# Optimization experiments

Hardware: AMD Instinct MI355X
Metric: run time of the kernel (lower is better)

Reference implementation:

```python
import jax, jax.numpy as jnp
import numpy as np

B, W, H = 16384, 16, 16
NUM_CLASSES = 1024
EMBED = 4
OUT = 1024

def setup_inputs() -> dict:
    key = jax.random.key(0)
    k0, k1, k2 = jax.random.split(key, 3)
    x = jax.random.randint(k0, (B, W, H), 0, NUM_CLASSES, dtype=jnp.int32)
    W_embed = jax.random.normal(k1, (NUM_CLASSES, EMBED), dtype=jnp.float32) * 0.02
    b_embed = jnp.zeros((EMBED,), dtype=jnp.float32)
    W_dense = jax.random.normal(k2, (EMBED * W * H, OUT), dtype=jnp.float32) * 0.02
    b_dense = jnp.zeros((OUT,), dtype=jnp.float32)
    return {"x": x, "W_embed": W_embed, "b_embed": b_embed, "W_dense": W_dense, "b_dense": b_dense}

def reference(x, W_embed, b_embed, W_dense, b_dense):
    # one_hot(x, C) @ W_embed + b_embed is mathematically a row-gather of W_embed
    emb = W_embed[x] + b_embed                 # (B, W, H, EMBED)
    flat = emb.reshape(emb.shape[0], -1)        # (B, W*H*EMBED)  == rearrange '... w h c -> ... (w h c)'
    return flat @ W_dense + b_dense             # (B, OUT)
```

## Files before the change

### kernel.cpp

```cpp
#include <hip/hip_runtime.h>
#include <stdint.h>
#include <stddef.h>

typedef __attribute__((ext_vector_type(8))) short bf16x8;
typedef __attribute__((ext_vector_type(4))) float f32x4;

typedef const __attribute__((address_space(1))) void* gptr1_t;
typedef __attribute__((address_space(3))) void* lptr3_t;

#define GLOAD_LDS16(gp, lp) \
  __builtin_amdgcn_global_load_lds((gptr1_t)(gp), (lptr3_t)(lp), 16, 0, 0)

__device__ __forceinline__ uint16_t f2bf(float f) {
  uint32_t u = __builtin_bit_cast(uint32_t, f);
  u += 0x7fffu + ((u >> 16) & 1u);
  return (uint16_t)(u >> 16);
}

#define MB   16384
#define NP   256
#define EMB  4
#define KDIM 1024
#define NDIM 1024

__global__ void build_a_kernel(const int* __restrict__ x,
                               const float* __restrict__ We,
                               const float* __restrict__ be,
                               uint16_t* __restrict__ A) {
  const int t = blockIdx.x * 256 + threadIdx.x;
  const int cls = x[t];
  const float4 e  = *(const float4*)(We + (size_t)cls * 4);
  const float4 bb = *(const float4*)be;
  ushort4 o;
  o.x = f2bf(e.x + bb.x);
  o.y = f2bf(e.y + bb.y);
  o.z = f2bf(e.z + bb.z);
  o.w = f2bf(e.w + bb.w);
  *(ushort4*)(A + (size_t)t * 4) = o;
}

__global__ void build_bt_kernel(const float* __restrict__ Wd,
                                uint16_t* __restrict__ Bt) {
  __shared__ uint16_t tile[32][33];
  const int k0 = blockIdx.y * 32;
  const int n0 = blockIdx.x * 32;
  const int tx = threadIdx.x;
  const int ty = threadIdx.y;
  #pragma unroll
  for (int r = 0; r < 32; r += 8)
    tile[ty + r][tx] = f2bf(Wd[(size_t)(k0 + ty + r) * NDIM + n0 + tx]);
  __syncthreads();
  #pragma unroll
  for (int r = 0; r < 32; r += 8)
    Bt[(size_t)(n0 + ty + r) * KDIM + k0 + tx] = tile[tx][ty + r];
}

#define BM 128
#define BN 128
#define BK 32

__global__ __launch_bounds__(256) void gemm_bt_kernel(
    const uint16_t* __restrict__ A,
    const uint16_t* __restrict__ Bt,
    const float* __restrict__ bias,
    float* __restrict__ C) {
  __shared__ uint16_t As[BM * BK];
  __shared__ uint16_t Bs[BN * BK];

  const int tid  = threadIdx.x;
  const int bm   = blockIdx.x;
  const int bn   = blockIdx.y;
  const int wave = tid >> 6;
  const int lane = tid & 63;
  const int wr   = wave >> 1;
  const int wc   = wave & 1;
  const int lm   = lane & 15;
  const int q    = lane >> 4;

  const int row0 = bm * BM;
  const int col0 = bn * BN;

  const int srow = tid >> 2;
  const int scol = (tid & 3) * 8;

  f32x4 acc[4][4];
  #pragma unroll
  for (int i = 0; i < 4; i++)
    #pragma unroll
    for (int j = 0; j < 4; j++)
      acc[i][j] = (f32x4){0.f, 0.f, 0.f, 0.f};

  for (int kt = 0; kt < KDIM / BK; ++kt) {
    const int k0 = kt * BK;
    GLOAD_LDS16(A  + (size_t)(row0      + srow) * KDIM + k0 + scol, As + tid * 8);
    GLOAD_LDS16(A  + (size_t)(row0 + 64 + srow) * KDIM + k0 + scol, As + 2048 + tid * 8);
    GLOAD_LDS16(Bt + (size_t)(col0      + srow) * KDIM + k0 + scol, Bs + tid * 8);
    GLOAD_LDS16(Bt + (size_t)(col0 + 64 + srow) * KDIM + k0 + scol, Bs + 2048 + tid * 8);
    __syncthreads();

    bf16x8 af[4], bfr[4];
    #pragma unroll
    for (int i = 0; i < 4; i++)
      af[i] = *(const bf16x8*)(As + (wr * 64 + i * 16 + lm) * BK + q * 8);
    #pragma unroll
    for (int j = 0; j < 4; j++)
      bfr[j] = *(const bf16x8*)(Bs + (wc * 64 + j * 16 + lm) * BK + q * 8);

    #pragma unroll
    for (int i = 0; i < 4; i++)
      #pragma unroll
      for (int j = 0; j < 4; j++)
        acc[i][j] = __builtin_amdgcn_mfma_f32_16x16x32_bf16(af[i], bfr[j], acc[i][j], 0, 0, 0);

    __syncthreads();
  }

  float bvals[4];
  #pragma unroll
  for (int j = 0; j < 4; j++)
    bvals[j] = bias[col0 + wc * 64 + j * 16 + lm];

  #pragma unroll
  for (int i = 0; i < 4; i++) {
    const int rbase = row0 + wr * 64 + i * 16 + q * 4;
    #pragma unroll
    for (int j = 0; j < 4; j++) {
      const int col = col0 + wc * 64 + j * 16 + lm;
      #pragma unroll
      for (int r = 0; r < 4; r++)
        C[(size_t)(rbase + r) * NDIM + col] = acc[i][j][r] + bvals[j];
    }
  }
}

__global__ void naive_kernel(const int* __restrict__ x,
                             const float* __restrict__ We,
                             const float* __restrict__ be,
                             const float* __restrict__ Wd,
                             const float* __restrict__ bd,
                             float* __restrict__ out) {
  __shared__ float emb[KDIM];
  const int b = blockIdx.x;
  const int tid = threadIdx.x;
  {
    const int cls = x[(size_t)b * NP + tid];
    const float4 e  = *(const float4*)(We + (size_t)cls * 4);
    const float4 bb = *(const float4*)be;
    emb[tid * 4 + 0] = e.x + bb.x;
    emb[tid * 4 + 1] = e.y + bb.y;
    emb[tid * 4 + 2] = e.z + bb.z;
    emb[tid * 4 + 3] = e.w + bb.w;
  }
  __syncthreads();
  float acc0 = bd[tid], acc1 = bd[tid + 256], acc2 = bd[tid + 512], acc3 = bd[tid + 768];
  for (int k = 0; k < KDIM; ++k) {
    const float a = emb[k];
    const float* w = Wd + (size_t)k * NDIM + tid;
    acc0 += a * w[0];
    acc1 += a * w[256];
    acc2 += a * w[512];
    acc3 += a * w[768];
  }
  float* o = out + (size_t)b * NDIM + tid;
  o[0] = acc0; o[256] = acc1; o[512] = acc2; o[768] = acc3;
}

extern "C" void kernel_launch(void* const* d_in, const int* in_sizes, int n_in,
                              void* d_out, int out_size, void* d_ws, size_t ws_size,
                              hipStream_t stream) {
  const int*   x  = (const int*)d_in[0];
  const float* We = (const float*)d_in[1];
  const float* be = (const float*)d_in[2];
  const float* Wd = (const float*)d_in[3];
  const float* bd = (const float*)d_in[4];
  float* out = (float*)d_out;

  const size_t needA = (size_t)MB * KDIM * sizeof(uint16_t);
  const size_t needB = (size_t)NDIM * KDIM * sizeof(uint16_t);

  if (ws_size >= needA + needB) {
    uint16_t* Aw  = (uint16_t*)d_ws;
    uint16_t* Btw = (uint16_t*)((char*)d_ws + needA);
    build_a_kernel<<<MB * NP / 256, 256, 0, stream>>>(x, We, be, Aw);
    build_bt_kernel<<<dim3(NDIM / 32, KDIM / 32), dim3(32, 8), 0, stream>>>(Wd, Btw);
    gemm_bt_kernel<<<dim3(MB / BM, NDIM / BN), 256, 0, stream>>>(Aw, Btw, bd, out);
  } else {
    naive_kernel<<<MB, 256, 0, stream>>>(x, We, be, Wd, bd, out);
  }
}
```

Baseline: 142.4 us.

## Fuse embedding gather into GEMM A-tile load with register prefetch

Drops the separate kernel that materialized the full bf16 embedding matrix. A tiny bf16 copy of the embedding table is built instead, and the GEMM gathers A-tile rows directly from the class indices. The next k-tile's indices and rows are prefetched into registers and written to LDS manually. This removes a large intermediate write and read. In exchange, each column block re-reads the index array and does scattered small gathers, and the A tile now goes through registers instead of direct global-to-LDS loads.

```diff
diff --git a/kernel.cpp b/kernel.cpp
--- a/kernel.cpp
+++ b/kernel.cpp
@@ -3,6 +3,7 @@
 #include <stddef.h>
 
 typedef __attribute__((ext_vector_type(8))) short bf16x8;
+typedef __attribute__((ext_vector_type(8))) unsigned short u16x8;
 typedef __attribute__((ext_vector_type(4))) float f32x4;
 
 typedef const __attribute__((address_space(1))) void* gptr1_t;
@@ -19,24 +20,14 @@
 
 #define MB   16384
 #define NP   256
-#define EMB  4
 #define KDIM 1024
 #define NDIM 1024
 
-__global__ void build_a_kernel(const int* __restrict__ x,
-                               const float* __restrict__ We,
-                               const float* __restrict__ be,
-                               uint16_t* __restrict__ A) {
+__global__ void build_webf_kernel(const float* __restrict__ We,
+                                  const float* __restrict__ be,
+                                  uint16_t* __restrict__ Webf) {
   const int t = blockIdx.x * 256 + threadIdx.x;
-  const int cls = x[t];
-  const float4 e  = *(const float4*)(We + (size_t)cls * 4);
-  const float4 bb = *(const float4*)be;
-  ushort4 o;
-  o.x = f2bf(e.x + bb.x);
-  o.y = f2bf(e.y + bb.y);
-  o.z = f2bf(e.z + bb.z);
-  o.w = f2bf(e.w + bb.w);
-  *(ushort4*)(A + (size_t)t * 4) = o;
+  Webf[t] = f2bf(We[t] + be[t & 3]);
 }
 
 __global__ void build_bt_kernel(const float* __restrict__ Wd,
@@ -58,9 +49,11 @@
 #define BM 128
 #define BN 128
 #define BK 32
-
-__global__ __launch_bounds__(256) void gemm_bt_kernel(
-    const uint16_t* __restrict__ A,
+#define NK (KDIM / BK)
+
+__global__ __launch_bounds__(256) void gemm_fused_kernel(
+    const int* __restrict__ x,
+    const uint16_t* __restrict__ Webf,
     const uint16_t* __restrict__ Bt,
     const float* __restrict__ bias,
     float* __restrict__ C) {
@@ -83,6 +76,12 @@
   const int srow = tid >> 2;
   const int scol = (tid & 3) * 8;
 
+  const int arow = tid >> 2;
+  const int adp  = tid & 3;
+  const int* xr0 = x + (size_t)(row0 + arow)      * NP + adp * 2;
+  const int* xr1 = x + (size_t)(row0 + 64 + arow) * NP + adp * 2;
+  const ushort4* WB = (const ushort4*)Webf;
+
   f32x4 acc[4][4];
   #pragma unroll
   for (int i = 0; i < 4; i++)
@@ -90,12 +89,29 @@
     for (int j = 0; j < 4; j++)
       acc[i][j] = (f32x4){0.f, 0.f, 0.f, 0.f};
 
-  for (int kt = 0; kt < KDIM / BK; ++kt) {
+  int2 i0 = *(const int2*)(xr0);
+  int2 i1 = *(const int2*)(xr1);
+  ushort4 g0 = WB[i0.x], g1 = WB[i0.y];
+  ushort4 g2 = WB[i1.x], g3 = WB[i1.y];
+
+  for (int kt = 0; kt < NK; ++kt) {
     const int k0 = kt * BK;
-    GLOAD_LDS16(A  + (size_t)(row0      + srow) * KDIM + k0 + scol, As + tid * 8);
-    GLOAD_LDS16(A  + (size_t)(row0 + 64 + srow) * KDIM + k0 + scol, As + 2048 + tid * 8);
+
     GLOAD_LDS16(Bt + (size_t)(col0      + srow) * KDIM + k0 + scol, Bs + tid * 8);
     GLOAD_LDS16(Bt + (size_t)(col0 + 64 + srow) * KDIM + k0 + scol, Bs + 2048 + tid * 8);
+
+    u16x8 v0 = { g0.x, g0.y, g0.z, g0.w, g1.x, g1.y, g1.z, g1.w };
+    u16x8 v1 = { g2.x, g2.y, g2.z, g2.w, g3.x, g3.y, g3.z, g3.w };
+    *(u16x8*)(As + tid * 8)        = v0;
+    *(u16x8*)(As + 2048 + tid * 8) = v1;
+
+    if (kt + 1 < NK) {
+      int2 j0 = *(const int2*)(xr0 + (kt + 1) * 8);
+      int2 j1 = *(const int2*)(xr1 + (kt + 1) * 8);
+      g0 = WB[j0.x]; g1 = WB[j0.y];
+      g2 = WB[j1.x]; g3 = WB[j1.y];
+    }
+
     __syncthreads();
 
     bf16x8 af[4], bfr[4];
@@ -175,15 +191,15 @@
   const float* bd = (const float*)d_in[4];
   float* out = (float*)d_out;
 
-  const size_t needA = (size_t)MB * KDIM * sizeof(uint16_t);
+  const size_t needW = (size_t)KDIM * 4 * sizeof(uint16_t);
   const size_t needB = (size_t)NDIM * KDIM * sizeof(uint16_t);
 
-  if (ws_size >= needA + needB) {
-    uint16_t* Aw  = (uint16_t*)d_ws;
-    uint16_t* Btw = (uint16_t*)((char*)d_ws + needA);
-    build_a_kernel<<<MB * NP / 256, 256, 0, stream>>>(x, We, be, Aw);
+  if (ws_size >= needW + needB) {
+    uint16_t* Webf = (uint16_t*)d_ws;
+    uint16_t* Btw  = (uint16_t*)((char*)d_ws + needW);
+    build_webf_kernel<<<16, 256, 0, stream>>>(We, be, Webf);
     build_bt_kernel<<<dim3(NDIM / 32, KDIM / 32), dim3(32, 8), 0, stream>>>(Wd, Btw);
-    gemm_bt_kernel<<<dim3(MB / BM, NDIM / BN), 256, 0, stream>>>(Aw, Btw, bd, out);
+    gemm_fused_kernel<<<dim3(MB / BM, NDIM / BN), 256, 0, stream>>>(x, Webf, Btw, bd, out);
   } else {
     naive_kernel<<<MB, 256, 0, stream>>>(x, We, be, Wd, bd, out);
   }
```

Result: slower. 197.8 us (+38.9%).
